# Optimization experiments

Measured on AMD Instinct MI355X. Metric: run time of the kernel, lower is better.

Reference implementation:

```python
import jax, jax.numpy as jnp
import numpy as np

N = 4096       # num nodes == output_dim (delta is symmetrized NxN)
E = 65536      # num edges (avg degree 16)
IN_DIM = 128
H = 256        # hidden_dim (channels)
HEADS = 4


def setup_inputs():
    key = jax.random.key(0)
    ks = iter(jax.random.split(key, 40))
    def w(shape, s=0.05):
        return jax.random.normal(next(ks), shape, jnp.float32) * s
    inp = {}
    inp['x'] = jax.random.normal(next(ks), (N, IN_DIM), jnp.float32)
    inp['edge_index'] = jax.random.randint(next(ks), (2, E), 0, N)
    inp['pre_w'] = w((H, IN_DIM)); inp['pre_b'] = w((H,))
    for p in ('g1', 'g2'):
        inp[p + '_gcn_w'] = w((H, H)); inp[p + '_gcn_b'] = w((H,))
        inp[p + '_attn_in_w'] = w((3 * H, H)); inp[p + '_attn_in_b'] = w((3 * H,))
        inp[p + '_attn_out_w'] = w((H, H)); inp[p + '_attn_out_b'] = w((H,))
        inp[p + '_ffn_w1'] = w((2 * H, H)); inp[p + '_ffn_b1'] = w((2 * H,))
        inp[p + '_ffn_w2'] = w((H, 2 * H)); inp[p + '_ffn_b2'] = w((H,))
    inp['mlp_w1'] = w((H, H)); inp['mlp_b1'] = w((H,))
    inp['mlp_w2'] = w((N, H)); inp['mlp_b2'] = w((N,))
    return inp


def _gcn(x, src, dst, W, b):
    n = x.shape[0]
    x = x @ W.T
    loop = jnp.arange(n)
    s = jnp.concatenate([src, loop])
    d = jnp.concatenate([dst, loop])
    deg = jax.ops.segment_sum(jnp.ones(s.shape[0], x.dtype), d, num_segments=n)
    dinv = jnp.where(deg > 0, jax.lax.rsqrt(deg), 0.0)
    coef = (dinv[s] * dinv[d])[:, None]
    out = jax.ops.segment_sum(x[s] * coef, d, num_segments=n)
    return out + b


def _mha(h, in_w, in_b, out_w, out_b):
    # nn.MultiheadAttention self-attention over all N nodes (single dense graph)
    n, c = h.shape
    d = c // HEADS
    qkv = h @ in_w.T + in_b                      # [N, 3C]
    q, k, v = jnp.split(qkv, 3, axis=-1)
    q = q.reshape(n, HEADS, d).transpose(1, 0, 2) * (d ** -0.5)  # [h, n, d]
    k = k.reshape(n, HEADS, d).transpose(1, 0, 2)
    v = v.reshape(n, HEADS, d).transpose(1, 0, 2)
    a = jax.nn.softmax(jnp.einsum('hnd,hmd->hnm', q, k), axis=-1)
    o = jnp.einsum('hnm,hmd->hnd', a, v).transpose(1, 0, 2).reshape(n, c)
    return o @ out_w.T + out_b


def _gps(x, src, dst, gw, gb, iw, ib, ow, ob, w1, b1, w2, b2):
    # GPSConv, eval mode: dropout off, batch_norm (default running stats) = identity
    h1 = _gcn(x, src, dst, gw, gb) + x
    h2 = _mha(x, iw, ib, ow, ob) + x
    out = h1 + h2
    ff = jax.nn.relu(out @ w1.T + b1) @ w2.T + b2
    return out + ff


def reference(x, edge_index, pre_w, pre_b,
              g1_gcn_w, g1_gcn_b, g1_attn_in_w, g1_attn_in_b, g1_attn_out_w, g1_attn_out_b,
              g1_ffn_w1, g1_ffn_b1, g1_ffn_w2, g1_ffn_b2,
              g2_gcn_w, g2_gcn_b, g2_attn_in_w, g2_attn_in_b, g2_attn_out_w, g2_attn_out_b,
              g2_ffn_w1, g2_ffn_b1, g2_ffn_w2, g2_ffn_b2,
              mlp_w1, mlp_b1, mlp_w2, mlp_b2):
    src, dst = edge_index[0], edge_index[1]
    h = jax.nn.relu(x @ pre_w.T + pre_b)
    h = jax.nn.relu(_gps(h, src, dst, g1_gcn_w, g1_gcn_b, g1_attn_in_w, g1_attn_in_b,
                         g1_attn_out_w, g1_attn_out_b, g1_ffn_w1, g1_ffn_b1, g1_ffn_w2, g1_ffn_b2))
    h = jax.nn.relu(_gps(h, src, dst, g2_gcn_w, g2_gcn_b, g2_attn_in_w, g2_attn_in_b,
                         g2_attn_out_w, g2_attn_out_b, g2_ffn_w1, g2_ffn_b1, g2_ffn_w2, g2_ffn_b2))
    delta = jax.nn.relu(h @ mlp_w1.T + mlp_b1) @ mlp_w2.T + mlp_b2  # [N, N]
    return (delta + delta.T) * 0.5
```

## Files before the change

kernel.cpp:

```cpp
#include <hip/hip_runtime.h>

#define NN 4096
#define EE 65536
#define HC 256

typedef unsigned short ushort_t;
typedef __attribute__((ext_vector_type(8))) short bf16x8;
typedef __attribute__((ext_vector_type(4))) float f32x4;

__device__ __forceinline__ ushort_t f2bf(float f) {
    unsigned int u = __float_as_uint(f);
    unsigned int r = (u + 0x7fffu + ((u >> 16) & 1u)) >> 16;
    return (ushort_t)r;
}
__device__ __forceinline__ float bf2f(ushort_t u) {
    return __uint_as_float(((unsigned int)u) << 16);
}

__global__ void deg_init_k(float* __restrict__ deg) {
    int i = blockIdx.x * 256 + threadIdx.x;
    deg[i] = 1.0f;
}
__global__ void deg_scatter_k(const int* __restrict__ dst, float* __restrict__ deg) {
    int e = blockIdx.x * 256 + threadIdx.x;
    atomicAdd(&deg[dst[e]], 1.0f);
}
__global__ void dinv_k(const float* __restrict__ deg, float* __restrict__ dinv) {
    int i = blockIdx.x * 256 + threadIdx.x;
    dinv[i] = rsqrtf(deg[i]);
}
__global__ __launch_bounds__(1024)
void scan_offsets_k(const float* __restrict__ deg, int* __restrict__ offs,
                    int* __restrict__ cursor) {
    __shared__ int part[1024];
    const int t = threadIdx.x;
    int c0 = (int)deg[t * 4 + 0] - 1;
    int c1 = (int)deg[t * 4 + 1] - 1;
    int c2 = (int)deg[t * 4 + 2] - 1;
    int c3 = (int)deg[t * 4 + 3] - 1;
    part[t] = c0 + c1 + c2 + c3;
    __syncthreads();
    for (int off = 1; off < 1024; off <<= 1) {
        int v = (t >= off) ? part[t - off] : 0;
        __syncthreads();
        part[t] += v;
        __syncthreads();
    }
    int base = (t == 0) ? 0 : part[t - 1];
    offs[t * 4 + 0] = base;
    offs[t * 4 + 1] = base + c0;
    offs[t * 4 + 2] = base + c0 + c1;
    offs[t * 4 + 3] = base + c0 + c1 + c2;
    cursor[t * 4 + 0] = base;
    cursor[t * 4 + 1] = base + c0;
    cursor[t * 4 + 2] = base + c0 + c1;
    cursor[t * 4 + 3] = base + c0 + c1 + c2;
    if (t == 1023) offs[4096] = part[1023];
}
__global__ void csr_fill_k(const int* __restrict__ src, const int* __restrict__ dst,
                           int* __restrict__ cursor, int* __restrict__ csr_src) {
    int e = blockIdx.x * 256 + threadIdx.x;
    int pos = atomicAdd(&cursor[dst[e]], 1);
    csr_src[pos] = src[e];
}

__global__ __launch_bounds__(256)
void gcn_gather_k(const float* __restrict__ xw, const float* __restrict__ dinv,
                  const int* __restrict__ offs, const int* __restrict__ csr_src,
                  float* __restrict__ agg) {
    const int node = blockIdx.x * 4 + (threadIdx.x >> 6);
    const int c = (threadIdx.x & 63) * 4;
    const float dd = dinv[node];
    float4 a = *(const float4*)&xw[(size_t)node * HC + c];
    const float self = dd * dd;
    float4 acc = make_float4(a.x * self, a.y * self, a.z * self, a.w * self);
    const int beg = offs[node], end = offs[node + 1];
    for (int e = beg; e < end; e++) {
        int s = csr_src[e];
        float coef = dinv[s] * dd;
        const float4 v = *(const float4*)&xw[(size_t)s * HC + c];
        acc.x += v.x * coef;
        acc.y += v.y * coef;
        acc.z += v.z * coef;
        acc.w += v.w * coef;
    }
    *(float4*)&agg[(size_t)node * HC + c] = acc;
}

__global__ void cvt_bf16_k(const float* __restrict__ in, ushort_t* __restrict__ out) {
    int i = (blockIdx.x * 256 + threadIdx.x) * 4;
    float4 v = *(const float4*)&in[i];
    ushort4 o;
    o.x = f2bf(v.x); o.y = f2bf(v.y); o.z = f2bf(v.z); o.w = f2bf(v.w);
    *(ushort4*)&out[i] = o;
}

__global__ __launch_bounds__(256)
void gemm_bf_k(const float* __restrict__ X, const float* __restrict__ W,
               const float* __restrict__ bias1, const float* __restrict__ bias2,
               const float* __restrict__ res1, const float* __restrict__ res2, float res2scale,
               float* __restrict__ out, int K, int M, int dorelu, int obf)
{
    __shared__ ushort_t As[64][72];
    __shared__ ushort_t Bs[64][72];
    const int t = threadIdx.x;
    const int w = t >> 6, lane = t & 63;
    const int m = lane & 15, quad = lane >> 4;
    const int row0 = blockIdx.y << 6, col0 = blockIdx.x << 6;
    const int sr = t >> 2;
    const int sc = (t & 3) << 4;

    f32x4 acc[4] = {};
    for (int k0 = 0; k0 < K; k0 += 64) {
        const float* xp = &X[(size_t)(row0 + sr) * K + k0 + sc];
        const float* wp = &W[(size_t)(col0 + sr) * K + k0 + sc];
        float4 xa = *(const float4*)xp,     xb = *(const float4*)(xp + 4);
        float4 xc = *(const float4*)(xp + 8), xd = *(const float4*)(xp + 12);
        float4 wa = *(const float4*)wp,     wb = *(const float4*)(wp + 4);
        float4 wc = *(const float4*)(wp + 8), wd = *(const float4*)(wp + 12);
        __syncthreads();
        {
            __attribute__((aligned(16))) ushort_t tx[16];
            tx[0]=f2bf(xa.x); tx[1]=f2bf(xa.y); tx[2]=f2bf(xa.z); tx[3]=f2bf(xa.w);
            tx[4]=f2bf(xb.x); tx[5]=f2bf(xb.y); tx[6]=f2bf(xb.z); tx[7]=f2bf(xb.w);
            tx[8]=f2bf(xc.x); tx[9]=f2bf(xc.y); tx[10]=f2bf(xc.z); tx[11]=f2bf(xc.w);
            tx[12]=f2bf(xd.x); tx[13]=f2bf(xd.y); tx[14]=f2bf(xd.z); tx[15]=f2bf(xd.w);
            *(uint4*)&As[sr][sc] = *(const uint4*)&tx[0];
            *(uint4*)&As[sr][sc + 8] = *(const uint4*)&tx[8];
            __attribute__((aligned(16))) ushort_t tw[16];
            tw[0]=f2bf(wa.x); tw[1]=f2bf(wa.y); tw[2]=f2bf(wa.z); tw[3]=f2bf(wa.w);
            tw[4]=f2bf(wb.x); tw[5]=f2bf(wb.y); tw[6]=f2bf(wb.z); tw[7]=f2bf(wb.w);
            tw[8]=f2bf(wc.x); tw[9]=f2bf(wc.y); tw[10]=f2bf(wc.z); tw[11]=f2bf(wc.w);
            tw[12]=f2bf(wd.x); tw[13]=f2bf(wd.y); tw[14]=f2bf(wd.z); tw[15]=f2bf(wd.w);
            *(uint4*)&Bs[sr][sc] = *(const uint4*)&tw[0];
            *(uint4*)&Bs[sr][sc + 8] = *(const uint4*)&tw[8];
        }
        __syncthreads();
        #pragma unroll
        for (int kc = 0; kc < 2; kc++) {
            bf16x8 af = *(const bf16x8*)&As[(w << 4) + m][kc * 32 + quad * 8];
            #pragma unroll
            for (int cb = 0; cb < 4; cb++) {
                bf16x8 bf = *(const bf16x8*)&Bs[cb * 16 + m][kc * 32 + quad * 8];
                acc[cb] = __builtin_amdgcn_mfma_f32_16x16x32_bf16(af, bf, acc[cb], 0, 0, 0);
            }
        }
    }
    #pragma unroll
    for (int cb = 0; cb < 4; cb++) {
        #pragma unroll
        for (int r = 0; r < 4; r++) {
            const int row = row0 + (w << 4) + quad * 4 + r;
            const int col = col0 + cb * 16 + m;
            float v = acc[cb][r];
            if (bias1) v += bias1[col];
            if (bias2) v += bias2[col];
            if (res1) v += res1[(size_t)row * M + col];
            if (res2) v += res2scale * res2[(size_t)row * M + col];
            if (dorelu) v = fmaxf(v, 0.f);
            if (obf) ((ushort_t*)out)[(size_t)row * M + col] = f2bf(v);
            else out[(size_t)row * M + col] = v;
        }
    }
}

__global__ __launch_bounds__(256)
void kv_prep_k(const float* __restrict__ qkv, ushort_t* __restrict__ Kb,
               ushort_t* __restrict__ Vtb)
{
    __shared__ ushort_t Vs[64][72];
    const int h = blockIdx.y;
    const int n0 = blockIdx.x << 6;
    const int t = threadIdx.x;
    for (int u = t; u < 1024; u += 256) {
        int r = u >> 4, c = u & 15;
        const float* kp = &qkv[(size_t)(n0 + r) * 768 + 256 + h * 64 + c * 4];
        float4 kv = *(const float4*)kp;
        float4 vv = *(const float4*)(kp + 256);
        ushort4 kb;
        kb.x = f2bf(kv.x); kb.y = f2bf(kv.y); kb.z = f2bf(kv.z); kb.w = f2bf(kv.w);
        *(ushort4*)&Kb[((size_t)(h * 4096 + n0 + r)) * 64 + c * 4] = kb;
        ushort4 vb;
        vb.x = f2bf(vv.x); vb.y = f2bf(vv.y); vb.z = f2bf(vv.z); vb.w = f2bf(vv.w);
        *(ushort4*)&Vs[r][c * 4] = vb;
    }
    __syncthreads();
    int d = t >> 2, kc = t & 3;
    __attribute__((aligned(16))) ushort_t vals[16];
    #pragma unroll
    for (int k = 0; k < 16; k++) vals[k] = Vs[kc * 16 + k][d];
    ushort_t* op = &Vtb[((size_t)(h * 64 + d)) * 4096 + n0 + kc * 16];
    *(uint4*)op = *(const uint4*)&vals[0];
    *(uint4*)(op + 8) = *(const uint4*)&vals[8];
}

__global__ __launch_bounds__(256)
void attn_part_k(const float* qkv, const ushort_t* __restrict__ Kb,
                 const ushort_t* __restrict__ Vtb, ushort_t* opart,
                 float* __restrict__ m_part, float* __restrict__ l_part)
{
    __shared__ ushort_t Kt[64][72];
    __shared__ ushort_t Vt[64][72];
    __shared__ ushort_t Plb[4][16][72];
    const int h = blockIdx.y & 3;
    const int split = blockIdx.y >> 2;
    const int q0 = blockIdx.x << 6;
    const int t = threadIdx.x;
    const int w = t >> 6, lane = t & 63;
    const int m = lane & 15, quad = lane >> 4;

    bf16x8 qf[2];
    #pragma unroll
    for (int kc = 0; kc < 2; kc++) {
        const float* qp = &qkv[(size_t)(q0 + w * 16 + m) * 768 + h * 64 + kc * 32 + quad * 8];
        float4 a = *(const float4*)qp;
        float4 b = *(const float4*)(qp + 4);
        qf[kc][0] = (short)f2bf(a.x * 0.125f);
        qf[kc][1] = (short)f2bf(a.y * 0.125f);
        qf[kc][2] = (short)f2bf(a.z * 0.125f);
        qf[kc][3] = (short)f2bf(a.w * 0.125f);
        qf[kc][4] = (short)f2bf(b.x * 0.125f);
        qf[kc][5] = (short)f2bf(b.y * 0.125f);
        qf[kc][6] = (short)f2bf(b.z * 0.125f);
        qf[kc][7] = (short)f2bf(b.w * 0.125f);
    }
    bf16x8 onesf;
    #pragma unroll
    for (int j = 0; j < 8; j++) onesf[j] = (short)0x3F80;

    f32x4 o[4], ol;
    float mrow[4];
    #pragma unroll
    for (int i = 0; i < 4; i++) {
        o[i] = (f32x4){0.f, 0.f, 0.f, 0.f};
        mrow[i] = -1e30f;
    }
    ol = (f32x4){0.f, 0.f, 0.f, 0.f};

    for (int kb = split * 16; kb < split * 16 + 16; kb++) {
        __syncthreads();
        for (int u = t; u < 512; u += 256) {
            int r = u >> 3, c = u & 7;
            *(uint4*)&Kt[r][c * 8] = *(const uint4*)&Kb[((size_t)(h * 4096 + kb * 64 + r)) * 64 + c * 8];
            *(uint4*)&Vt[r][c * 8] = *(const uint4*)&Vtb[((size_t)(h * 64 + r)) * 4096 + kb * 64 + c * 8];
        }
        __syncthreads();

        f32x4 s[4];
        #pragma unroll
        for (int b = 0; b < 4; b++) s[b] = (f32x4){0.f, 0.f, 0.f, 0.f};
        #pragma unroll
        for (int b = 0; b < 4; b++)
            #pragma unroll
            for (int kc = 0; kc < 2; kc++) {
                bf16x8 kf = *(const bf16x8*)&Kt[b * 16 + m][kc * 32 + quad * 8];
                s[b] = __builtin_amdgcn_mfma_f32_16x16x32_bf16(qf[kc], kf, s[b], 0, 0, 0);
            }

        #pragma unroll
        for (int r = 0; r < 4; r++) {
            float mx = fmaxf(fmaxf(s[0][r], s[1][r]), fmaxf(s[2][r], s[3][r]));
            #pragma unroll
            for (int off = 1; off < 16; off <<= 1)
                mx = fmaxf(mx, __shfl_xor(mx, off));
            float mn = fmaxf(mrow[r], mx);
            float alpha = __expf(mrow[r] - mn);
            mrow[r] = mn;
            #pragma unroll
            for (int b = 0; b < 4; b++)
                Plb[w][quad * 4 + r][b * 16 + m] = f2bf(__expf(s[b][r] - mn));
            o[0][r] *= alpha; o[1][r] *= alpha;
            o[2][r] *= alpha; o[3][r] *= alpha;
            ol[r] *= alpha;
        }

        #pragma unroll
        for (int kc = 0; kc < 2; kc++) {
            bf16x8 pa = *(const bf16x8*)&Plb[w][m][kc * 32 + quad * 8];
            #pragma unroll
            for (int nb = 0; nb < 4; nb++) {
                bf16x8 vf = *(const bf16x8*)&Vt[nb * 16 + m][kc * 32 + quad * 8];
                o[nb] = __builtin_amdgcn_mfma_f32_16x16x32_bf16(pa, vf, o[nb], 0, 0, 0);
            }
            ol = __builtin_amdgcn_mfma_f32_16x16x32_bf16(pa, onesf, ol, 0, 0, 0);
        }
    }

    #pragma unroll
    for (int nb = 0; nb < 4; nb++)
        #pragma unroll
        for (int r = 0; r < 4; r++) {
            int q = q0 + w * 16 + quad * 4 + r;
            opart[(size_t)q * 1536 + 512 + split * 256 + h * 64 + nb * 16 + m] = f2bf(o[nb][r]);
        }
    if (m == 0) {
        #pragma unroll
        for (int r = 0; r < 4; r++) {
            int q = q0 + w * 16 + quad * 4 + r;
            m_part[(split * 4 + h) * 4096 + q] = mrow[r];
            l_part[(split * 4 + h) * 4096 + q] = ol[r];
        }
    }
}

__global__ __launch_bounds__(256)
void attn_merge_k(const ushort_t* __restrict__ opart, const float* __restrict__ m_part,
                  const float* __restrict__ l_part, float* __restrict__ att)
{
    int idx = blockIdx.x * 256 + threadIdx.x;
    int q = idx >> 8, c = idx & 255;
    int h = c >> 6, d = c & 63;
    float ms[4];
    float mmax = -1e30f;
    #pragma unroll
    for (int s = 0; s < 4; s++) {
        ms[s] = m_part[(s * 4 + h) * 4096 + q];
        mmax = fmaxf(mmax, ms[s]);
    }
    float onum = 0.f, lden = 0.f;
    #pragma unroll
    for (int s = 0; s < 4; s++) {
        float wgt = __expf(ms[s] - mmax);
        float ov = bf2f(opart[(size_t)q * 1536 + 512 + s * 256 + h * 64 + d]);
        onum += wgt * ov;
        lden += wgt * l_part[(s * 4 + h) * 4096 + q];
    }
    att[(size_t)q * 256 + c] = onum / lden;
}

__global__ __launch_bounds__(256)
void sym_mlp_mfma_k(const ushort_t* __restrict__ Tb, const ushort_t* __restrict__ Wb,
                    const float* __restrict__ b2, float* __restrict__ out)
{
    __shared__ ushort_t As[128][72];
    __shared__ ushort_t Bs[128][72];
    const int t = threadIdx.x;
    const int w = t >> 6, lane = t & 63;
    const int m = lane & 15, quad = lane >> 4;
    const int wr = (w >> 1) * 64, wc = (w & 1) * 64;
    const int ri = blockIdx.y * 128, rj = blockIdx.x * 128;

    f32x4 acc[4][4] = {};
    for (int kk = 0; kk < 8; kk++) {
        const int k0 = kk * 64;
        const ushort_t* Asrc = (k0 < 256) ? Tb : Wb;
        const ushort_t* Bsrc = (k0 < 256) ? Wb : Tb;
        const int kcol = k0 & 255;
        __syncthreads();
        #pragma unroll
        for (int i = 0; i < 4; i++) {
            int s = t + i * 256;
            int row = s >> 3, ch = (s & 7) * 8;
            *(uint4*)&As[row][ch] = *(const uint4*)&Asrc[(size_t)(ri + row) * 256 + kcol + ch];
            *(uint4*)&Bs[row][ch] = *(const uint4*)&Bsrc[(size_t)(rj + row) * 256 + kcol + ch];
        }
        __syncthreads();
        #pragma unroll
        for (int kc = 0; kc < 2; kc++) {
            bf16x8 af[4], bfr[4];
            #pragma unroll
            for (int rb = 0; rb < 4; rb++)
                af[rb] = *(const bf16x8*)&As[wr + rb * 16 + m][kc * 32 + quad * 8];
            #pragma unroll
            for (int cb = 0; cb < 4; cb++)
                bfr[cb] = *(const bf16x8*)&Bs[wc + cb * 16 + m][kc * 32 + quad * 8];
            #pragma unroll
            for (int rb = 0; rb < 4; rb++)
                #pragma unroll
                for (int cb = 0; cb < 4; cb++)
                    acc[rb][cb] = __builtin_amdgcn_mfma_f32_16x16x32_bf16(af[rb], bfr[cb], acc[rb][cb], 0, 0, 0);
        }
    }
    #pragma unroll
    for (int rb = 0; rb < 4; rb++) {
        #pragma unroll
        for (int r = 0; r < 4; r++) {
            const int gr = ri + wr + rb * 16 + quad * 4 + r;
            const float br = b2[gr];
            #pragma unroll
            for (int cb = 0; cb < 4; cb++) {
                const int gc = rj + wc + cb * 16 + m;
                out[(size_t)gr * NN + gc] = 0.5f * (acc[rb][cb][r] + br + b2[gc]);
            }
        }
    }
}

extern "C" void kernel_launch(void* const* d_in, const int* in_sizes, int n_in,
                              void* d_out, int out_size, void* d_ws, size_t ws_size,
                              hipStream_t stream) {
    (void)in_sizes; (void)n_in; (void)out_size; (void)ws_size;
    const float* x = (const float*)d_in[0];
    const int* ei = (const int*)d_in[1];
    const int* src = ei;
    const int* dst = ei + EE;

    float* ws = (float*)d_ws;
    const int NH = NN * HC;
    float* h0  = ws;
    float* hb  = ws + 1 * NH;
    float* hc  = ws + 2 * NH;
    float* att = ws + 3 * NH;
    float* qkv = ws + 4 * NH;
    float* ffh = ws + 4 * NH;
    float* deg = ws + 7 * NH;
    float* dinv = deg + NN;
    int* offs    = (int*)(dinv + NN);
    int* cursor  = offs + 4100;
    int* csr_src = cursor + 4096;
    float* m_part = (float*)(csr_src + EE);
    float* l_part = m_part + 65536;
    ushort_t* Kb  = (ushort_t*)hc;
    ushort_t* Vtb = Kb + NH;
    ushort_t* Tb  = (ushort_t*)hb;
    ushort_t* W2b = Tb + NH;

    deg_init_k<<<NN / 256, 256, 0, stream>>>(deg);
    deg_scatter_k<<<EE / 256, 256, 0, stream>>>(dst, deg);
    dinv_k<<<NN / 256, 256, 0, stream>>>(deg, dinv);
    scan_offsets_k<<<1, 1024, 0, stream>>>(deg, offs, cursor);
    csr_fill_k<<<EE / 256, 256, 0, stream>>>(src, dst, cursor, csr_src);

    gemm_bf_k<<<dim3(4, 64), 256, 0, stream>>>(
        x, (const float*)d_in[2], (const float*)d_in[3], nullptr,
        nullptr, nullptr, 0.f, h0, 128, 256, 1, 0);

    for (int L = 0; L < 2; L++) {
        int B = 4 + L * 10;
        const float* gw = (const float*)d_in[B + 0];
        const float* gb = (const float*)d_in[B + 1];
        const float* iw = (const float*)d_in[B + 2];
        const float* ib = (const float*)d_in[B + 3];
        const float* ow = (const float*)d_in[B + 4];
        const float* ob = (const float*)d_in[B + 5];
        const float* w1 = (const float*)d_in[B + 6];
        const float* b1 = (const float*)d_in[B + 7];
        const float* w2 = (const float*)d_in[B + 8];
        const float* b2 = (const float*)d_in[B + 9];

        gemm_bf_k<<<dim3(4, 64), 256, 0, stream>>>(
            h0, gw, nullptr, nullptr, nullptr, nullptr, 0.f, att, 256, 256, 0, 0);
        gcn_gather_k<<<NN / 4, 256, 0, stream>>>(att, dinv, offs, csr_src, hb);
        gemm_bf_k<<<dim3(12, 64), 256, 0, stream>>>(
            h0, iw, ib, nullptr, nullptr, nullptr, 0.f, qkv, 256, 768, 0, 0);
        kv_prep_k<<<dim3(64, 4), 256, 0, stream>>>(qkv, Kb, Vtb);
        attn_part_k<<<dim3(64, 16), 256, 0, stream>>>(
            qkv, Kb, Vtb, (ushort_t*)qkv, m_part, l_part);
        attn_merge_k<<<NN, 256, 0, stream>>>(
            (const ushort_t*)qkv, m_part, l_part, att);
        gemm_bf_k<<<dim3(4, 64), 256, 0, stream>>>(
            att, ow, ob, gb, hb, h0, 2.0f, hc, 256, 256, 0, 0);
        gemm_bf_k<<<dim3(8, 64), 256, 0, stream>>>(
            hc, w1, b1, nullptr, nullptr, nullptr, 0.f, ffh, 256, 512, 1, 0);
        gemm_bf_k<<<dim3(4, 64), 256, 0, stream>>>(
            ffh, w2, b2, nullptr, hc, nullptr, 0.f, h0, 512, 256, 1, 0);
    }

    gemm_bf_k<<<dim3(4, 64), 256, 0, stream>>>(
        h0, (const float*)d_in[24], (const float*)d_in[25], nullptr,
        nullptr, nullptr, 0.f, (float*)Tb, 256, 256, 1, 1);
    cvt_bf16_k<<<NH / 1024, 256, 0, stream>>>((const float*)d_in[26], W2b);
    sym_mlp_mfma_k<<<dim3(32, 32), 256, 0, stream>>>(
        Tb, W2b, (const float*)d_in[27], (float*)d_out);
}
```

Baseline: 494.1 us.

## Merge GCN and QKV projections into one GEMM launch, cheaper bf16 packing

Runs the GCN weight projection and the QKV in-projection as one column-split GEMM launch, since both read the same h0 input. This removes one kernel launch per layer and fills the GPU with a larger grid. It also replaces per-element round-to-nearest-even bf16 conversion with a pack-two-at-a-time add-and-permute, which rounds ties away from zero and slightly changes numerics. In the attention kernel, P is now written with vectorized stores in a permuted column order, and K rows are loaded with a matching permutation so the results stay consistent.

```diff
diff --git a/kernel.cpp b/kernel.cpp
--- a/kernel.cpp
+++ b/kernel.cpp
@@ -15,6 +15,11 @@
 }
 __device__ __forceinline__ float bf2f(ushort_t u) {
     return __uint_as_float(((unsigned int)u) << 16);
+}
+__device__ __forceinline__ unsigned int pack2bf(float a, float b) {
+    unsigned int ua = __float_as_uint(a) + 0x8000u;
+    unsigned int ub = __float_as_uint(b) + 0x8000u;
+    return __builtin_amdgcn_perm(ub, ua, 0x07060302u);
 }
 
 __global__ void deg_init_k(float* __restrict__ deg) {
@@ -90,16 +95,17 @@
 __global__ void cvt_bf16_k(const float* __restrict__ in, ushort_t* __restrict__ out) {
     int i = (blockIdx.x * 256 + threadIdx.x) * 4;
     float4 v = *(const float4*)&in[i];
-    ushort4 o;
-    o.x = f2bf(v.x); o.y = f2bf(v.y); o.z = f2bf(v.z); o.w = f2bf(v.w);
-    *(ushort4*)&out[i] = o;
+    unsigned int d0 = pack2bf(v.x, v.y), d1 = pack2bf(v.z, v.w);
+    *(uint2*)&out[i] = make_uint2(d0, d1);
 }
 
 __global__ __launch_bounds__(256)
 void gemm_bf_k(const float* __restrict__ X, const float* __restrict__ W,
                const float* __restrict__ bias1, const float* __restrict__ bias2,
                const float* __restrict__ res1, const float* __restrict__ res2, float res2scale,
-               float* __restrict__ out, int K, int M, int dorelu, int obf)
+               float* __restrict__ out, int K, int M, int dorelu, int obf,
+               int colsplit, const float* __restrict__ W2,
+               const float* __restrict__ bias_r2, float* __restrict__ out2, int M2)
 {
     __shared__ ushort_t As[64][72];
     __shared__ ushort_t Bs[64][72];
@@ -110,30 +116,40 @@
     const int sr = t >> 2;
     const int sc = (t & 3) << 4;
 
+    const float* Wu = W;
+    const float* b1u = bias1;
+    const float* b2u = bias2;
+    float* outu = out;
+    int Mu = M, colu = col0;
+    if (colsplit > 0 && col0 >= colsplit) {
+        Wu = W2; b1u = bias_r2; b2u = nullptr;
+        outu = out2; Mu = M2; colu = col0 - colsplit;
+    }
+
     f32x4 acc[4] = {};
     for (int k0 = 0; k0 < K; k0 += 64) {
         const float* xp = &X[(size_t)(row0 + sr) * K + k0 + sc];
-        const float* wp = &W[(size_t)(col0 + sr) * K + k0 + sc];
-        float4 xa = *(const float4*)xp,     xb = *(const float4*)(xp + 4);
+        const float* wp = &Wu[(size_t)(colu + sr) * K + k0 + sc];
+        float4 xa = *(const float4*)xp,       xb = *(const float4*)(xp + 4);
         float4 xc = *(const float4*)(xp + 8), xd = *(const float4*)(xp + 12);
-        float4 wa = *(const float4*)wp,     wb = *(const float4*)(wp + 4);
+        float4 wa = *(const float4*)wp,       wb = *(const float4*)(wp + 4);
         float4 wc = *(const float4*)(wp + 8), wd = *(const float4*)(wp + 12);
         __syncthreads();
         {
-            __attribute__((aligned(16))) ushort_t tx[16];
-            tx[0]=f2bf(xa.x); tx[1]=f2bf(xa.y); tx[2]=f2bf(xa.z); tx[3]=f2bf(xa.w);
-            tx[4]=f2bf(xb.x); tx[5]=f2bf(xb.y); tx[6]=f2bf(xb.z); tx[7]=f2bf(xb.w);
-            tx[8]=f2bf(xc.x); tx[9]=f2bf(xc.y); tx[10]=f2bf(xc.z); tx[11]=f2bf(xc.w);
-            tx[12]=f2bf(xd.x); tx[13]=f2bf(xd.y); tx[14]=f2bf(xd.z); tx[15]=f2bf(xd.w);
-            *(uint4*)&As[sr][sc] = *(const uint4*)&tx[0];
-            *(uint4*)&As[sr][sc + 8] = *(const uint4*)&tx[8];
-            __attribute__((aligned(16))) ushort_t tw[16];
-            tw[0]=f2bf(wa.x); tw[1]=f2bf(wa.y); tw[2]=f2bf(wa.z); tw[3]=f2bf(wa.w);
-            tw[4]=f2bf(wb.x); tw[5]=f2bf(wb.y); tw[6]=f2bf(wb.z); tw[7]=f2bf(wb.w);
-            tw[8]=f2bf(wc.x); tw[9]=f2bf(wc.y); tw[10]=f2bf(wc.z); tw[11]=f2bf(wc.w);
-            tw[12]=f2bf(wd.x); tw[13]=f2bf(wd.y); tw[14]=f2bf(wd.z); tw[15]=f2bf(wd.w);
-            *(uint4*)&Bs[sr][sc] = *(const uint4*)&tw[0];
-            *(uint4*)&Bs[sr][sc + 8] = *(const uint4*)&tw[8];
+            unsigned int tx[8];
+            tx[0] = pack2bf(xa.x, xa.y); tx[1] = pack2bf(xa.z, xa.w);
+            tx[2] = pack2bf(xb.x, xb.y); tx[3] = pack2bf(xb.z, xb.w);
+            tx[4] = pack2bf(xc.x, xc.y); tx[5] = pack2bf(xc.z, xc.w);
+            tx[6] = pack2bf(xd.x, xd.y); tx[7] = pack2bf(xd.z, xd.w);
+            *(uint4*)&As[sr][sc]     = *(const uint4*)&tx[0];
+            *(uint4*)&As[sr][sc + 8] = *(const uint4*)&tx[4];
+            unsigned int tw[8];
+            tw[0] = pack2bf(wa.x, wa.y); tw[1] = pack2bf(wa.z, wa.w);
+            tw[2] = pack2bf(wb.x, wb.y); tw[3] = pack2bf(wb.z, wb.w);
+            tw[4] = pack2bf(wc.x, wc.y); tw[5] = pack2bf(wc.z, wc.w);
+            tw[6] = pack2bf(wd.x, wd.y); tw[7] = pack2bf(wd.z, wd.w);
+            *(uint4*)&Bs[sr][sc]     = *(const uint4*)&tw[0];
+            *(uint4*)&Bs[sr][sc + 8] = *(const uint4*)&tw[4];
         }
         __syncthreads();
         #pragma unroll
@@ -151,15 +167,15 @@
         #pragma unroll
         for (int r = 0; r < 4; r++) {
             const int row = row0 + (w << 4) + quad * 4 + r;
-            const int col = col0 + cb * 16 + m;
+            const int col = colu + cb * 16 + m;
             float v = acc[cb][r];
-            if (bias1) v += bias1[col];
-            if (bias2) v += bias2[col];
-            if (res1) v += res1[(size_t)row * M + col];
-            if (res2) v += res2scale * res2[(size_t)row * M + col];
+            if (b1u) v += b1u[col];
+            if (b2u) v += b2u[col];
+            if (res1) v += res1[(size_t)row * Mu + col];
+            if (res2) v += res2scale * res2[(size_t)row * Mu + col];
             if (dorelu) v = fmaxf(v, 0.f);
-            if (obf) ((ushort_t*)out)[(size_t)row * M + col] = f2bf(v);
-            else out[(size_t)row * M + col] = v;
+            if (obf) ((ushort_t*)outu)[(size_t)row * Mu + col] = f2bf(v);
+            else outu[(size_t)row * Mu + col] = v;
         }
     }
 }
@@ -177,12 +193,10 @@
         const float* kp = &qkv[(size_t)(n0 + r) * 768 + 256 + h * 64 + c * 4];
         float4 kv = *(const float4*)kp;
         float4 vv = *(const float4*)(kp + 256);
-        ushort4 kb;
-        kb.x = f2bf(kv.x); kb.y = f2bf(kv.y); kb.z = f2bf(kv.z); kb.w = f2bf(kv.w);
-        *(ushort4*)&Kb[((size_t)(h * 4096 + n0 + r)) * 64 + c * 4] = kb;
-        ushort4 vb;
-        vb.x = f2bf(vv.x); vb.y = f2bf(vv.y); vb.z = f2bf(vv.z); vb.w = f2bf(vv.w);
-        *(ushort4*)&Vs[r][c * 4] = vb;
+        *(uint2*)&Kb[((size_t)(h * 4096 + n0 + r)) * 64 + c * 4] =
+            make_uint2(pack2bf(kv.x, kv.y), pack2bf(kv.z, kv.w));
+        *(uint2*)&Vs[r][c * 4] =
+            make_uint2(pack2bf(vv.x, vv.y), pack2bf(vv.z, vv.w));
     }
     __syncthreads();
     int d = t >> 2, kc = t & 3;
@@ -241,7 +255,8 @@
         __syncthreads();
         for (int u = t; u < 512; u += 256) {
             int r = u >> 3, c = u & 7;
-            *(uint4*)&Kt[r][c * 8] = *(const uint4*)&Kb[((size_t)(h * 4096 + kb * 64 + r)) * 64 + c * 8];
+            int pr = ((r & 15) << 2) | (r >> 4);
+            *(uint4*)&Kt[r][c * 8] = *(const uint4*)&Kb[((size_t)(h * 4096 + kb * 64 + pr)) * 64 + c * 8];
             *(uint4*)&Vt[r][c * 8] = *(const uint4*)&Vtb[((size_t)(h * 64 + r)) * 4096 + kb * 64 + c * 8];
         }
         __syncthreads();
@@ -266,9 +281,9 @@
             float mn = fmaxf(mrow[r], mx);
             float alpha = __expf(mrow[r] - mn);
             mrow[r] = mn;
-            #pragma unroll
-            for (int b = 0; b < 4; b++)
-                Plb[w][quad * 4 + r][b * 16 + m] = f2bf(__expf(s[b][r] - mn));
+            unsigned int d0 = pack2bf(__expf(s[0][r] - mn), __expf(s[1][r] - mn));
+            unsigned int d1 = pack2bf(__expf(s[2][r] - mn), __expf(s[3][r] - mn));
+            *(uint2*)&Plb[w][quad * 4 + r][m * 4] = make_uint2(d0, d1);
             o[0][r] *= alpha; o[1][r] *= alpha;
             o[2][r] *= alpha; o[3][r] *= alpha;
             ol[r] *= alpha;
@@ -423,7 +438,8 @@
 
     gemm_bf_k<<<dim3(4, 64), 256, 0, stream>>>(
         x, (const float*)d_in[2], (const float*)d_in[3], nullptr,
-        nullptr, nullptr, 0.f, h0, 128, 256, 1, 0);
+        nullptr, nullptr, 0.f, h0, 128, 256, 1, 0,
+        0, nullptr, nullptr, nullptr, 0);
 
     for (int L = 0; L < 2; L++) {
         int B = 4 + L * 10;
@@ -438,27 +454,30 @@
         const float* w2 = (const float*)d_in[B + 8];
         const float* b2 = (const float*)d_in[B + 9];
 
-        gemm_bf_k<<<dim3(4, 64), 256, 0, stream>>>(
-            h0, gw, nullptr, nullptr, nullptr, nullptr, 0.f, att, 256, 256, 0, 0);
+        gemm_bf_k<<<dim3(16, 64), 256, 0, stream>>>(
+            h0, gw, nullptr, nullptr, nullptr, nullptr, 0.f, att, 256, 256, 0, 0,
+            256, iw, ib, qkv, 768);
         gcn_gather_k<<<NN / 4, 256, 0, stream>>>(att, dinv, offs, csr_src, hb);
-        gemm_bf_k<<<dim3(12, 64), 256, 0, stream>>>(
-            h0, iw, ib, nullptr, nullptr, nullptr, 0.f, qkv, 256, 768, 0, 0);
         kv_prep_k<<<dim3(64, 4), 256, 0, stream>>>(qkv, Kb, Vtb);
         attn_part_k<<<dim3(64, 16), 256, 0, stream>>>(
             qkv, Kb, Vtb, (ushort_t*)qkv, m_part, l_part);
         attn_merge_k<<<NN, 256, 0, stream>>>(
             (const ushort_t*)qkv, m_part, l_part, att);
         gemm_bf_k<<<dim3(4, 64), 256, 0, stream>>>(
-            att, ow, ob, gb, hb, h0, 2.0f, hc, 256, 256, 0, 0);
+            att, ow, ob, gb, hb, h0, 2.0f, hc, 256, 256, 0, 0,
+            0, nullptr, nullptr, nullptr, 0);
         gemm_bf_k<<<dim3(8, 64), 256, 0, stream>>>(
-            hc, w1, b1, nullptr, nullptr, nullptr, 0.f, ffh, 256, 512, 1, 0);
+            hc, w1, b1, nullptr, nullptr, nullptr, 0.f, ffh, 256, 512, 1, 0,
+            0, nullptr, nullptr, nullptr, 0);
         gemm_bf_k<<<dim3(4, 64), 256, 0, stream>>>(
-            ffh, w2, b2, nullptr, hc, nullptr, 0.f, h0, 512, 256, 1, 0);
+            ffh, w2, b2, nullptr, hc, nullptr, 0.f, h0, 512, 256, 1, 0,
+            0, nullptr, nullptr, nullptr, 0);
     }
 
     gemm_bf_k<<<dim3(4, 64), 256, 0, stream>>>(
         h0, (const float*)d_in[24], (const float*)d_in[25], nullptr,
-        nullptr, nullptr, 0.f, (float*)Tb, 256, 256, 1, 1);
+        nullptr, nullptr, 0.f, (float*)Tb, 256, 256, 1, 1,
+        0, nullptr, nullptr, nullptr, 0);
     cvt_bf16_k<<<NH / 1024, 256, 0, stream>>>((const float*)d_in[26], W2b);
     sym_mlp_mfma_k<<<dim3(32, 32), 256, 0, stream>>>(
         Tb, W2b, (const float*)d_in[27], (float*)d_out);
```

Measured after the change: 466.0 us. 5.7% less time.
